# Optimization experiments

Measured on AMD Instinct MI355X. Metric: run time of the kernel, lower is better.

## Reference

```python
import jax, jax.numpy as jnp
import numpy as np

H = 32          # heads
E = 32          # head dim = mdl_channels // heads (must equal heads per module bug)
C = 1024        # mdl_channels == in_channels
MAXP = 128      # max_position_embeddings
EPS = 1e-5


def _layernorm(x, g, b):
    mu = jnp.mean(x, axis=-1, keepdims=True)
    var = jnp.var(x, axis=-1, keepdims=True)
    return (x - mu) * jax.lax.rsqrt(var + EPS) * g + b


def setup_inputs() -> dict:
    key = jax.random.key(0)
    ks = jax.random.split(key, 16)
    s = 0.02
    N, L = 4, 1024
    inp = {
        "x": jax.random.normal(ks[0], (N, L, C), jnp.float32),
        "Wq": jax.random.normal(ks[1], (C, C), jnp.float32) * s,
        "bq": jnp.zeros((C,), jnp.float32),
        "Wk": jax.random.normal(ks[2], (C, C), jnp.float32) * s,
        "bk": jnp.zeros((C,), jnp.float32),
        "Wv": jax.random.normal(ks[3], (C, C), jnp.float32) * s,
        "bv": jnp.zeros((C,), jnp.float32),
        "dist_emb": jax.random.normal(ks[4], (2 * MAXP + 1, E), jnp.float32) * s,
        "ln1_g": jnp.ones((C,), jnp.float32),
        "ln1_b": jnp.zeros((C,), jnp.float32),
        "ln2_g": jnp.ones((C,), jnp.float32),
        "ln2_b": jnp.zeros((C,), jnp.float32),
        "W1": jax.random.normal(ks[5], (C, C), jnp.float32) * s,
        "b1": jnp.zeros((C,), jnp.float32),
        "W2": jax.random.normal(ks[6], (C, C), jnp.float32) * s,
        "b2": jnp.zeros((C,), jnp.float32),
    }
    return inp


def reference(x, Wq, bq, Wk, bk, Wv, bv, dist_emb, ln1_g, ln1_b,
              ln2_g, ln2_b, W1, b1, W2, b2):
    N, L, _ = x.shape
    # QKV projections -> (N, L, H, E)
    q = (x @ Wq + bq).reshape(N, L, H, E)
    k = (x @ Wk + bk).reshape(N, L, H, E)
    v = (x @ Wv + bv).reshape(N, L, H, E)

    temp = 1.0 / np.sqrt(E).astype(np.float32)
    # content scores (N, H, L, S)
    QK = jnp.einsum('nlhe,nshe->nhls', q, k)
    # relative position scores (disentangled attention)
    pos = jnp.arange(L)
    dist = jnp.clip(pos[:, None] - pos[None, :], -MAXP, MAXP) + MAXP  # (L, L)
    pe = dist_emb[dist]                                              # (L, L, E)
    QK = QK + jnp.einsum('nlhe,lse->nhls', q, pe) \
            + jnp.einsum('nshe,lse->nhls', k, pe)
    A = jax.nn.softmax(temp * QK, axis=-1)          # dropout: eval mode (identity)
    t = jnp.einsum('nhls,nshe->nlhe', A, v).reshape(N, L, C)

    h = _layernorm(t + x, ln1_g, ln1_b)             # AddNorm (attention)
    m = jax.nn.relu(h @ W1 + b1) @ W2 + b2          # 2-layer MLP
    out = _layernorm(m + h, ln2_g, ln2_b)           # AddNorm (mlp)
    return jnp.swapaxes(out, 0, 1)                  # 'n f c -> f n c'
```

## Files before the change

### kernel.cpp

```cpp
#include <hip/hip_runtime.h>

#define H_ 32
#define E_ 32
#define C_ 1024
#define L_ 1024
#define N_ 4
#define M_ 4096
#define NH_ 128
#define D_ 257
#define QDP 264
#define TEMP_ 0.17677669529663687f
#define QSCALE_ (TEMP_ * 1.4426950408889634f)

typedef unsigned short u16;
typedef __attribute__((ext_vector_type(8))) short short8;
typedef __attribute__((ext_vector_type(4))) float f32x4;
typedef __attribute__((ext_vector_type(4))) unsigned short u16x4;

__device__ __forceinline__ u16 f2bf(float f) {
  union { float f; unsigned u; } v; v.f = f;
  unsigned r = v.u + 0x7fffu + ((v.u >> 16) & 1u);
  return (u16)(r >> 16);
}
__device__ __forceinline__ float bf2f(u16 h) {
  union { unsigned u; float f; } v; v.u = ((unsigned)h) << 16;
  return v.f;
}
__device__ __forceinline__ f32x4 mfma16(short8 a, short8 b, f32x4 c) {
  return __builtin_amdgcn_mfma_f32_16x16x32_bf16(a, b, c, 0, 0, 0);
}
__device__ __forceinline__ float exp2a(float x) {
  float r;
  asm("v_exp_f32 %0, %1\n\ts_nop 1" : "=v"(r) : "v"(x));
  return r;
}
__device__ __forceinline__ void gld16(const u16* g, u16* l) {
  __builtin_amdgcn_global_load_lds(
      (const __attribute__((address_space(1))) unsigned int*)g,
      (__attribute__((address_space(3))) unsigned int*)l, 16, 0, 0);
}

__global__ __launch_bounds__(256) void prep_kernel(
    const float* __restrict__ demb, const float* __restrict__ bq,
    const float* __restrict__ bk, const float* __restrict__ bv,
    u16* __restrict__ demb_b, float* __restrict__ bqkv) {
  int i = blockIdx.x * 256 + threadIdx.x;
  if (i < D_ * E_) demb_b[i] = f2bf(demb[i]);
  if (i < C_) { bqkv[i] = bq[i]; bqkv[C_ + i] = bk[i]; bqkv[2 * C_ + i] = bv[i]; }
}

__global__ __launch_bounds__(256) void cvt_x_kernel(const float* __restrict__ x,
                                                    u16* __restrict__ xb) {
  int i = blockIdx.x * 256 + threadIdx.x;
  f32x4 v = reinterpret_cast<const f32x4*>(x)[i];
  u16x4 o2;
  o2[0] = f2bf(v[0]); o2[1] = f2bf(v[1]); o2[2] = f2bf(v[2]); o2[3] = f2bf(v[3]);
  reinterpret_cast<u16x4*>(xb)[i] = o2;
}

__global__ __launch_bounds__(256) void transpose_w_kernel(const float* __restrict__ in,
                                                          u16* __restrict__ out) {
  __shared__ float tile[32][33];
  int j0 = blockIdx.x * 32, c0 = blockIdx.y * 32;
#pragma unroll
  for (int i = 0; i < 4; ++i) {
    int cy = threadIdx.y + i * 8;
    tile[cy][threadIdx.x] = in[(size_t)(c0 + cy) * C_ + j0 + threadIdx.x];
  }
  __syncthreads();
#pragma unroll
  for (int i = 0; i < 4; ++i) {
    int jy = threadIdx.y + i * 8;
    out[(size_t)(j0 + jy) * C_ + c0 + threadIdx.x] = f2bf(tile[threadIdx.x][jy]);
  }
}

template <int EPI>
__global__ __launch_bounds__(256) void gemm128_kernel(
    const u16* __restrict__ A, const u16* __restrict__ Bt, int K,
    const float* __restrict__ bias,
    u16* __restrict__ out0, u16* __restrict__ out1, u16* __restrict__ out2) {
  __shared__ u16 As[128 * 64];
  __shared__ u16 Bs[128 * 64];
  const int bid = blockIdx.x;
  const int m0 = (bid & 31) << 7;
  const int n0 = (bid >> 5) << 7;
  const int tid = threadIdx.x;
  const int w = tid >> 6, lane = tid & 63, lhi = lane >> 4, llo = lane & 15;
  const int wr = w >> 1, wc = w & 1;
  const int w4 = w << 2;
  const int srow = lane >> 3, scol = (lane & 7) << 3;
  f32x4 acc[4][4] = {};
  for (int k0 = 0; k0 < K; k0 += 64) {
#pragma unroll
    for (int j = 0; j < 4; ++j) {
      const int seg = w4 + j;
      const int row = (seg << 3) + srow;
      gld16(&A[(size_t)(m0 + row) * K + k0 + scol], &As[seg << 9]);
      gld16(&Bt[(size_t)(n0 + row) * K + k0 + scol], &Bs[seg << 9]);
    }
    __syncthreads();
#pragma unroll
    for (int kk = 0; kk < 2; ++kk) {
      const int ko = (kk << 5) + lhi * 8;
      short8 af[4], bf[4];
#pragma unroll
      for (int mi = 0; mi < 4; ++mi)
        af[mi] = *reinterpret_cast<const short8*>(&As[(wr * 64 + mi * 16 + llo) * 64 + ko]);
#pragma unroll
      for (int ni = 0; ni < 4; ++ni)
        bf[ni] = *reinterpret_cast<const short8*>(&Bs[(wc * 64 + ni * 16 + llo) * 64 + ko]);
#pragma unroll
      for (int mi = 0; mi < 4; ++mi)
#pragma unroll
        for (int ni = 0; ni < 4; ++ni)
          acc[mi][ni] = mfma16(af[mi], bf[ni], acc[mi][ni]);
    }
    __syncthreads();
  }
#pragma unroll
  for (int mi = 0; mi < 4; ++mi)
#pragma unroll
    for (int ni = 0; ni < 4; ++ni)
#pragma unroll
      for (int r = 0; r < 4; ++r) {
        int row = m0 + wr * 64 + mi * 16 + lhi * 4 + r;
        int col = n0 + wc * 64 + ni * 16 + llo;
        float v = acc[mi][ni][r] + bias[col];
        if constexpr (EPI == 0) {
          int which = col >> 10, jj = col & 1023, h = jj >> 5, e2 = jj & 31;
          int n = row >> 10, l = row & 1023;
          int nh = (n << 5) | h;
          if (which == 0) v *= QSCALE_;
          u16 bvv = f2bf(v);
          if (which == 0)      out0[((size_t)((nh << 10) | l)) * 32 + e2] = bvv;
          else if (which == 1) out1[((size_t)((nh << 10) | l)) * 32 + e2] = bvv;
          else                 out2[(((size_t)(nh * 32 + e2)) << 10) | l] = bvv;
        } else if constexpr (EPI == 1) {
          out0[(size_t)row * C_ + col] = f2bf(fmaxf(v, 0.f));
        } else {
          out0[(size_t)row * C_ + col] = f2bf(v);
        }
      }
}

__global__ __launch_bounds__(256) void qdkd_kernel(
    const u16* __restrict__ src, const u16* __restrict__ demb,
    u16* __restrict__ dst, int dstride, float scale,
    u16* __restrict__ aux0, u16* __restrict__ aux256) {
  const int wt = blockIdx.x * 4 + (threadIdx.x >> 6);
  const int lane = threadIdx.x & 63, lhi = lane >> 4, llo = lane & 15;
  const int m0 = wt << 4;
  short8 a = *reinterpret_cast<const short8*>(&src[(size_t)(m0 + llo) * E_ + lhi * 8]);
#pragma unroll
  for (int ct = 0; ct < 17; ++ct) {
    int d = ct * 16 + llo;
    short8 b = {0, 0, 0, 0, 0, 0, 0, 0};
    if (d < D_) b = *reinterpret_cast<const short8*>(&demb[d * E_ + lhi * 8]);
    f32x4 c = {};
    c = mfma16(a, b, c);
    if (d < D_) {
#pragma unroll
      for (int r = 0; r < 4; ++r) {
        u16 val = f2bf(c[r] * scale);
        dst[(size_t)(m0 + lhi * 4 + r) * dstride + d] = val;
        if (aux0 != nullptr && d == 0)     aux0[m0 + lhi * 4 + r] = val;
        if (aux256 != nullptr && d == 256) aux256[m0 + lhi * 4 + r] = val;
      }
    }
  }
}

__global__ __launch_bounds__(256) void attn_kernel(
    const u16* __restrict__ qw, const u16* __restrict__ kw,
    const u16* __restrict__ vT, const u16* __restrict__ QDg,
    const u16* __restrict__ KDg, const u16* __restrict__ kd0a,
    const u16* __restrict__ kd256a, u16* __restrict__ tb) {
  __shared__ u16 QDs[64 * QDP];
  __shared__ u16 kdc[2 * 1024];
  __shared__ u16 Pbuf[4 * 16 * 40];
  __shared__ float Lred[64];
  const int bid = blockIdx.x;
  const int nh = bid >> 4;
  const int l0 = (bid & 15) << 6;
  const int tid = threadIdx.x;
  const int w = tid >> 6, lane = tid & 63, lhi = lane >> 4, llo = lane & 15;
  const int lw0 = l0 + (w << 4);

  const u16* qb  = qw + (size_t)nh * (L_ * E_);
  const u16* kb  = kw + (size_t)nh * (L_ * E_);
  const u16* vb  = vT + (size_t)nh * (E_ * L_);
  const u16* qdg = QDg + (size_t)nh * ((size_t)L_ * QDP);
  const u16* kdg = KDg + (size_t)nh * ((size_t)L_ * D_);

  {
    const int rr = tid >> 2, q4 = tid & 3;
#pragma unroll
    for (int j = 0; j < 9; ++j) {
      int c = q4 + j * 4;
      if (c < 33)
        *reinterpret_cast<short8*>(&QDs[rr * QDP + c * 8]) =
            *reinterpret_cast<const short8*>(&qdg[(size_t)(l0 + rr) * QDP + c * 8]);
    }
    const int side = tid >> 7, off = (tid & 127) * 8;
    const u16* srcA = (side ? kd256a : kd0a) + (size_t)nh * L_ + off;
    *reinterpret_cast<short8*>(&kdc[side * 1024 + off]) =
        *reinterpret_cast<const short8*>(srcA);
  }
  __syncthreads();

  const short8 qA = *reinterpret_cast<const short8*>(&qb[(size_t)(lw0 + llo) * E_ + lhi * 8]);
  const int qr4 = (w << 4) + (lhi << 2);
  float qdf0[4], qdf256[4];
#pragma unroll
  for (int r = 0; r < 4; ++r) {
    qdf0[r]   = bf2f(QDs[(qr4 + r) * QDP + 0]);
    qdf256[r] = bf2f(QDs[(qr4 + r) * QDP + 256]);
  }

  u16* Pw = &Pbuf[w * 16 * 40];
  f32x4 o0 = {}, o1 = {};
  float lacc[4] = {0.f, 0.f, 0.f, 0.f};

  for (int s0 = 0; s0 < L_; s0 += 32) {
    short8 kB0 = *reinterpret_cast<const short8*>(&kb[(size_t)(s0 + llo) * E_ + lhi * 8]);
    short8 kB1 = *reinterpret_cast<const short8*>(&kb[(size_t)(s0 + 16 + llo) * E_ + lhi * 8]);
    f32x4 st0 = {}, st1 = {};
    st0 = mfma16(qA, kB0, st0);
    st1 = mfma16(qA, kB1, st1);

    const int dmin = lw0 - s0 - 31, dmax = lw0 + 15 - s0;
    float p0[4], p1[4];
    if (dmin >= 128 || dmax <= -128) {
      const int sd = (dmin >= 128) ? 1 : 0;
      const float* qdf = sd ? qdf256 : qdf0;
      const float kc0 = bf2f(kdc[sd * 1024 + s0 + llo]);
      const float kc1 = bf2f(kdc[sd * 1024 + s0 + 16 + llo]);
#pragma unroll
      for (int r = 0; r < 4; ++r) {
        p0[r] = exp2a(st0[r] + qdf[r] + kc0);
        p1[r] = exp2a(st1[r] + qdf[r] + kc1);
      }
    } else if (dmin >= -128 && dmax <= 128) {
      const int sc0 = s0 + llo, sc1 = s0 + 16 + llo;
      u16x4 kd0v = *reinterpret_cast<const u16x4*>(&kdg[256 * sc0 + lw0 + (lhi << 2) + 128]);
      u16x4 kd1v = *reinterpret_cast<const u16x4*>(&kdg[256 * sc1 + lw0 + (lhi << 2) + 128]);
#pragma unroll
      for (int r = 0; r < 4; ++r) {
        const int qq = lw0 + (lhi << 2) + r;
        float qd0 = bf2f(QDs[(qr4 + r) * QDP + (qq - sc0 + 128)]);
        float qd1 = bf2f(QDs[(qr4 + r) * QDP + (qq - sc1 + 128)]);
        p0[r] = exp2a(st0[r] + qd0 + bf2f(kd0v[r]));
        p1[r] = exp2a(st1[r] + qd1 + bf2f(kd1v[r]));
      }
    } else {
#pragma unroll
      for (int r = 0; r < 4; ++r) {
        const int qq = lw0 + (lhi << 2) + r;
        int d0 = qq - (s0 + llo);
        d0 = (d0 < -128 ? -128 : (d0 > 128 ? 128 : d0)) + 128;
        int d1 = qq - (s0 + 16 + llo);
        d1 = (d1 < -128 ? -128 : (d1 > 128 ? 128 : d1)) + 128;
        float qd0 = bf2f(QDs[(qr4 + r) * QDP + d0]);
        float qd1 = bf2f(QDs[(qr4 + r) * QDP + d1]);
        float kd0 = bf2f(kdg[(size_t)(s0 + llo) * D_ + d0]);
        float kd1 = bf2f(kdg[(size_t)(s0 + 16 + llo) * D_ + d1]);
        p0[r] = exp2a(st0[r] + qd0 + kd0);
        p1[r] = exp2a(st1[r] + qd1 + kd1);
      }
    }

#pragma unroll
    for (int r = 0; r < 4; ++r) {
      lacc[r] += p0[r] + p1[r];
      union { float f; unsigned u; } a0, a1; a0.f = p0[r]; a1.f = p1[r];
      const int prow = ((lhi << 2) + r) * 40;
      Pw[prow + llo]      = (u16)((a0.u + 0x8000u) >> 16);
      Pw[prow + 16 + llo] = (u16)((a1.u + 0x8000u) >> 16);
    }
    short8 pB = *reinterpret_cast<const short8*>(&Pw[llo * 40 + lhi * 8]);
    short8 vA0 = *reinterpret_cast<const short8*>(&vb[(size_t)llo * L_ + s0 + lhi * 8]);
    short8 vA1 = *reinterpret_cast<const short8*>(&vb[(size_t)(16 + llo) * L_ + s0 + lhi * 8]);
    o0 = mfma16(vA0, pB, o0);
    o1 = mfma16(vA1, pB, o1);
  }

#pragma unroll
  for (int r = 0; r < 4; ++r) {
    float t = lacc[r];
    t += __shfl_xor(t, 1); t += __shfl_xor(t, 2);
    t += __shfl_xor(t, 4); t += __shfl_xor(t, 8);
    if (llo == 0) Lred[(w << 4) + (lhi << 2) + r] = t;
  }
  const float inv = 1.0f / Lred[(w << 4) + llo];

  const int n = nh >> 5, h = nh & 31;
  const size_t obase = (((size_t)((n << 10) | (lw0 + llo))) * 32 + h) * 32;
  u16x4 w0, w1;
#pragma unroll
  for (int r = 0; r < 4; ++r) {
    w0[r] = f2bf(o0[r] * inv);
    w1[r] = f2bf(o1[r] * inv);
  }
  *reinterpret_cast<u16x4*>(&tb[obase + (lhi << 2)]) = w0;
  *reinterpret_cast<u16x4*>(&tb[obase + 16 + (lhi << 2)]) = w1;
}

__global__ __launch_bounds__(256) void ln1_kernel(
    const u16* __restrict__ tbuf, const float* __restrict__ x,
    const float* __restrict__ g, const float* __restrict__ b,
    u16* __restrict__ hb) {
  __shared__ float red[8];
  const int row = blockIdx.x, tid = threadIdx.x;
  const size_t base = (size_t)row * C_ + tid * 4;
  f32x4 xv = *reinterpret_cast<const f32x4*>(&x[base]);
  u16x4 tv = *reinterpret_cast<const u16x4*>(&tbuf[base]);
  float v[4]; float s1 = 0.f, s2 = 0.f;
#pragma unroll
  for (int i = 0; i < 4; ++i) {
    v[i] = xv[i] + bf2f(tv[i]);
    s1 += v[i]; s2 += v[i] * v[i];
  }
#pragma unroll
  for (int off = 32; off >= 1; off >>= 1) {
    s1 += __shfl_xor(s1, off); s2 += __shfl_xor(s2, off);
  }
  if ((tid & 63) == 0) { red[tid >> 6] = s1; red[4 + (tid >> 6)] = s2; }
  __syncthreads();
  float S1 = red[0] + red[1] + red[2] + red[3];
  float S2 = red[4] + red[5] + red[6] + red[7];
  float mu = S1 * (1.f / C_);
  float rs = rsqrtf(S2 * (1.f / C_) - mu * mu + 1e-5f);
#pragma unroll
  for (int i = 0; i < 4; ++i) {
    int c = tid * 4 + i;
    hb[base + i] = f2bf((v[i] - mu) * rs * g[c] + b[c]);
  }
}

__global__ __launch_bounds__(256) void ln2_kernel(
    const u16* __restrict__ mb, const u16* __restrict__ hb,
    const float* __restrict__ g, const float* __restrict__ b,
    float* __restrict__ out) {
  __shared__ float red[8];
  const int row = blockIdx.x, tid = threadIdx.x;
  const size_t base = (size_t)row * C_ + tid * 4;
  u16x4 mv = *reinterpret_cast<const u16x4*>(&mb[base]);
  u16x4 hv = *reinterpret_cast<const u16x4*>(&hb[base]);
  float v[4]; float s1 = 0.f, s2 = 0.f;
#pragma unroll
  for (int i = 0; i < 4; ++i) {
    v[i] = bf2f(mv[i]) + bf2f(hv[i]);
    s1 += v[i]; s2 += v[i] * v[i];
  }
#pragma unroll
  for (int off = 32; off >= 1; off >>= 1) {
    s1 += __shfl_xor(s1, off); s2 += __shfl_xor(s2, off);
  }
  if ((tid & 63) == 0) { red[tid >> 6] = s1; red[4 + (tid >> 6)] = s2; }
  __syncthreads();
  float S1 = red[0] + red[1] + red[2] + red[3];
  float S2 = red[4] + red[5] + red[6] + red[7];
  float mu = S1 * (1.f / C_);
  float rs = rsqrtf(S2 * (1.f / C_) - mu * mu + 1e-5f);
  const int n = row >> 10, l = row & 1023;
  const size_t ob = (size_t)(l * N_ + n) * C_ + tid * 4;
#pragma unroll
  for (int i = 0; i < 4; ++i) {
    int c = tid * 4 + i;
    out[ob + i] = (v[i] - mu) * rs * g[c] + b[c];
  }
}

extern "C" void kernel_launch(void* const* d_in, const int* in_sizes, int n_in,
                              void* d_out, int out_size, void* d_ws, size_t ws_size,
                              hipStream_t stream) {
  const float* x    = (const float*)d_in[0];
  const float* Wq   = (const float*)d_in[1];
  const float* bq   = (const float*)d_in[2];
  const float* Wk   = (const float*)d_in[3];
  const float* bk   = (const float*)d_in[4];
  const float* Wv   = (const float*)d_in[5];
  const float* bv   = (const float*)d_in[6];
  const float* demb = (const float*)d_in[7];
  const float* g1   = (const float*)d_in[8];
  const float* b1ln = (const float*)d_in[9];
  const float* g2   = (const float*)d_in[10];
  const float* b2ln = (const float*)d_in[11];
  const float* W1   = (const float*)d_in[12];
  const float* b1   = (const float*)d_in[13];
  const float* W2   = (const float*)d_in[14];
  const float* b2   = (const float*)d_in[15];
  float* outp = (float*)d_out;

  size_t o = 0;
  auto alloc = [&](size_t bytes) { size_t r = o; o += (bytes + 255) & ~(size_t)255; return r; };
  const size_t xb_o    = alloc((size_t)M_ * C_ * 2);
  const size_t wqkv_o  = alloc((size_t)3 * C_ * C_ * 2);
  const size_t w1_o    = alloc((size_t)C_ * C_ * 2);
  const size_t w2_o    = alloc((size_t)C_ * C_ * 2);
  const size_t bqkv_o  = alloc((size_t)3 * C_ * 4);
  const size_t demb_o  = alloc((size_t)D_ * E_ * 2);
  const size_t q_o     = alloc((size_t)NH_ * L_ * E_ * 2);
  const size_t k_o     = alloc((size_t)NH_ * L_ * E_ * 2);
  const size_t vt_o    = alloc((size_t)NH_ * L_ * E_ * 2);
  const size_t qd_o    = alloc((size_t)NH_ * L_ * QDP * 2);
  const size_t kd_o    = alloc((size_t)NH_ * L_ * D_ * 2);
  const size_t kd0_o   = alloc((size_t)NH_ * L_ * 2);
  const size_t kd256_o = alloc((size_t)NH_ * L_ * 2);
  const size_t t_o     = alloc((size_t)M_ * C_ * 2);
  const size_t h_o     = alloc((size_t)M_ * C_ * 2);
  const size_t m1_o    = alloc((size_t)M_ * C_ * 2);
  const size_t m_o     = alloc((size_t)M_ * C_ * 2);
  if (o > ws_size) return;

  char* ws = (char*)d_ws;
  u16*   xb     = (u16*)(ws + xb_o);
  u16*   wqkv_t = (u16*)(ws + wqkv_o);
  u16*   w1_t   = (u16*)(ws + w1_o);
  u16*   w2_t   = (u16*)(ws + w2_o);
  float* bqkv   = (float*)(ws + bqkv_o);
  u16*   demb_b = (u16*)(ws + demb_o);
  u16*   q_ws   = (u16*)(ws + q_o);
  u16*   k_ws   = (u16*)(ws + k_o);
  u16*   vT_ws  = (u16*)(ws + vt_o);
  u16*   QD     = (u16*)(ws + qd_o);
  u16*   KD     = (u16*)(ws + kd_o);
  u16*   kd0a   = (u16*)(ws + kd0_o);
  u16*   kd256a = (u16*)(ws + kd256_o);
  u16*   t_b16  = (u16*)(ws + t_o);
  u16*   h_b16  = (u16*)(ws + h_o);
  u16*   m1_b16 = (u16*)(ws + m1_o);
  u16*   m_b16  = (u16*)(ws + m_o);

  prep_kernel<<<33, 256, 0, stream>>>(demb, bq, bk, bv, demb_b, bqkv);
  cvt_x_kernel<<<(M_ * C_) / 1024, 256, 0, stream>>>(x, xb);
  dim3 tb_(32, 8), tg_(32, 32);
  transpose_w_kernel<<<tg_, tb_, 0, stream>>>(Wq, wqkv_t);
  transpose_w_kernel<<<tg_, tb_, 0, stream>>>(Wk, wqkv_t + (size_t)C_ * C_);
  transpose_w_kernel<<<tg_, tb_, 0, stream>>>(Wv, wqkv_t + (size_t)2 * C_ * C_);
  transpose_w_kernel<<<tg_, tb_, 0, stream>>>(W1, w1_t);
  transpose_w_kernel<<<tg_, tb_, 0, stream>>>(W2, w2_t);

  gemm128_kernel<0><<<32 * 24, 256, 0, stream>>>(xb, wqkv_t, C_, bqkv, q_ws, k_ws, vT_ws);

  qdkd_kernel<<<2048, 256, 0, stream>>>(q_ws, demb_b, QD, QDP, 1.0f, nullptr, nullptr);
  qdkd_kernel<<<2048, 256, 0, stream>>>(k_ws, demb_b, KD, D_, QSCALE_, kd0a, kd256a);

  attn_kernel<<<NH_ * 16, 256, 0, stream>>>(q_ws, k_ws, vT_ws, QD, KD, kd0a, kd256a, t_b16);

  ln1_kernel<<<M_, 256, 0, stream>>>(t_b16, x, g1, b1ln, h_b16);

  gemm128_kernel<1><<<32 * 8, 256, 0, stream>>>(h_b16, w1_t, C_, b1, m1_b16, nullptr, nullptr);
  gemm128_kernel<2><<<32 * 8, 256, 0, stream>>>(m1_b16, w2_t, C_, b2, m_b16, nullptr, nullptr);

  ln2_kernel<<<M_, 256, 0, stream>>>(m_b16, h_b16, g2, b2ln, outp);
}
```

Before: 321.7 us.

## Fuse Q·demb into attention, merge prep kernels, interleave key columns

New measurement: 311.8 us. 3.1% less time.

```diff
diff --git a/kernel.cpp b/kernel.cpp
--- a/kernel.cpp
+++ b/kernel.cpp
@@ -8,6 +8,7 @@
 #define M_ 4096
 #define NH_ 128
 #define D_ 257
+#define DPAD 272
 #define QDP 264
 #define TEMP_ 0.17677669529663687f
 #define QSCALE_ (TEMP_ * 1.4426950408889634f)
@@ -29,10 +30,14 @@
 __device__ __forceinline__ f32x4 mfma16(short8 a, short8 b, f32x4 c) {
   return __builtin_amdgcn_mfma_f32_16x16x32_bf16(a, b, c, 0, 0, 0);
 }
-__device__ __forceinline__ float exp2a(float x) {
+__device__ __forceinline__ float ex2(float x) {
+#if __has_builtin(__builtin_amdgcn_exp2f)
+  return __builtin_amdgcn_exp2f(x);
+#else
   float r;
   asm("v_exp_f32 %0, %1\n\ts_nop 1" : "=v"(r) : "v"(x));
   return r;
+#endif
 }
 __device__ __forceinline__ void gld16(const u16* g, u16* l) {
   __builtin_amdgcn_global_load_lds(
@@ -40,27 +45,33 @@
       (__attribute__((address_space(3))) unsigned int*)l, 16, 0, 0);
 }
 
-__global__ __launch_bounds__(256) void prep_kernel(
-    const float* __restrict__ demb, const float* __restrict__ bq,
-    const float* __restrict__ bk, const float* __restrict__ bv,
+__global__ __launch_bounds__(256) void misc_kernel(
+    const float* __restrict__ x, const float* __restrict__ demb,
+    const float* __restrict__ bq, const float* __restrict__ bk,
+    const float* __restrict__ bv, u16* __restrict__ xb,
     u16* __restrict__ demb_b, float* __restrict__ bqkv) {
-  int i = blockIdx.x * 256 + threadIdx.x;
-  if (i < D_ * E_) demb_b[i] = f2bf(demb[i]);
-  if (i < C_) { bqkv[i] = bq[i]; bqkv[C_ + i] = bk[i]; bqkv[2 * C_ + i] = bv[i]; }
-}
-
-__global__ __launch_bounds__(256) void cvt_x_kernel(const float* __restrict__ x,
-                                                    u16* __restrict__ xb) {
-  int i = blockIdx.x * 256 + threadIdx.x;
-  f32x4 v = reinterpret_cast<const f32x4*>(x)[i];
-  u16x4 o2;
-  o2[0] = f2bf(v[0]); o2[1] = f2bf(v[1]); o2[2] = f2bf(v[2]); o2[3] = f2bf(v[3]);
-  reinterpret_cast<u16x4*>(xb)[i] = o2;
-}
-
-__global__ __launch_bounds__(256) void transpose_w_kernel(const float* __restrict__ in,
-                                                          u16* __restrict__ out) {
+  const int b = blockIdx.x, tid = threadIdx.x;
+  if (b < 4096) {
+    int i = b * 256 + tid;
+    f32x4 v = reinterpret_cast<const f32x4*>(x)[i];
+    u16x4 o2;
+    o2[0] = f2bf(v[0]); o2[1] = f2bf(v[1]); o2[2] = f2bf(v[2]); o2[3] = f2bf(v[3]);
+    reinterpret_cast<u16x4*>(xb)[i] = o2;
+  } else {
+    int i = (b - 4096) * 256 + tid;
+    if (i < DPAD * E_) demb_b[i] = (i < D_ * E_) ? f2bf(demb[i]) : (u16)0;
+    if (i < C_) { bqkv[i] = bq[i]; bqkv[C_ + i] = bk[i]; bqkv[2 * C_ + i] = bv[i]; }
+  }
+}
+
+__global__ __launch_bounds__(256) void transpose_w_kernel(
+    const float* __restrict__ Wq, const float* __restrict__ Wk,
+    const float* __restrict__ Wv, const float* __restrict__ W1,
+    const float* __restrict__ W2, u16* __restrict__ out_base) {
   __shared__ float tile[32][33];
+  const int z = blockIdx.z;
+  const float* in = (z == 0) ? Wq : (z == 1) ? Wk : (z == 2) ? Wv : (z == 3) ? W1 : W2;
+  u16* out = out_base + (size_t)z * C_ * C_;
   int j0 = blockIdx.x * 32, c0 = blockIdx.y * 32;
 #pragma unroll
   for (int i = 0; i < 4; ++i) {
@@ -146,8 +157,7 @@
 
 __global__ __launch_bounds__(256) void qdkd_kernel(
     const u16* __restrict__ src, const u16* __restrict__ demb,
-    u16* __restrict__ dst, int dstride, float scale,
-    u16* __restrict__ aux0, u16* __restrict__ aux256) {
+    u16* __restrict__ dst, u16* __restrict__ aux0, u16* __restrict__ aux256) {
   const int wt = blockIdx.x * 4 + (threadIdx.x >> 6);
   const int lane = threadIdx.x & 63, lhi = lane >> 4, llo = lane & 15;
   const int m0 = wt << 4;
@@ -162,10 +172,10 @@
     if (d < D_) {
 #pragma unroll
       for (int r = 0; r < 4; ++r) {
-        u16 val = f2bf(c[r] * scale);
-        dst[(size_t)(m0 + lhi * 4 + r) * dstride + d] = val;
-        if (aux0 != nullptr && d == 0)     aux0[m0 + lhi * 4 + r] = val;
-        if (aux256 != nullptr && d == 256) aux256[m0 + lhi * 4 + r] = val;
+        u16 val = f2bf(c[r] * QSCALE_);
+        dst[(size_t)(m0 + lhi * 4 + r) * D_ + d] = val;
+        if (d == 0)   aux0[m0 + lhi * 4 + r] = val;
+        if (d == 256) aux256[m0 + lhi * 4 + r] = val;
       }
     }
   }
@@ -173,7 +183,7 @@
 
 __global__ __launch_bounds__(256) void attn_kernel(
     const u16* __restrict__ qw, const u16* __restrict__ kw,
-    const u16* __restrict__ vT, const u16* __restrict__ QDg,
+    const u16* __restrict__ vT, const u16* __restrict__ dembp,
     const u16* __restrict__ KDg, const u16* __restrict__ kd0a,
     const u16* __restrict__ kd256a, u16* __restrict__ tb) {
   __shared__ u16 QDs[64 * QDP];
@@ -181,8 +191,8 @@
   __shared__ u16 Pbuf[4 * 16 * 40];
   __shared__ float Lred[64];
   const int bid = blockIdx.x;
-  const int nh = bid >> 4;
-  const int l0 = (bid & 15) << 6;
+  const int nh = bid & (NH_ - 1);
+  const int l0 = (bid >> 7) << 6;
   const int tid = threadIdx.x;
   const int w = tid >> 6, lane = tid & 63, lhi = lane >> 4, llo = lane & 15;
   const int lw0 = l0 + (w << 4);
@@ -190,26 +200,29 @@
   const u16* qb  = qw + (size_t)nh * (L_ * E_);
   const u16* kb  = kw + (size_t)nh * (L_ * E_);
   const u16* vb  = vT + (size_t)nh * (E_ * L_);
-  const u16* qdg = QDg + (size_t)nh * ((size_t)L_ * QDP);
   const u16* kdg = KDg + (size_t)nh * ((size_t)L_ * D_);
 
   {
-    const int rr = tid >> 2, q4 = tid & 3;
-#pragma unroll
-    for (int j = 0; j < 9; ++j) {
-      int c = q4 + j * 4;
-      if (c < 33)
-        *reinterpret_cast<short8*>(&QDs[rr * QDP + c * 8]) =
-            *reinterpret_cast<const short8*>(&qdg[(size_t)(l0 + rr) * QDP + c * 8]);
-    }
     const int side = tid >> 7, off = (tid & 127) * 8;
     const u16* srcA = (side ? kd256a : kd0a) + (size_t)nh * L_ + off;
     *reinterpret_cast<short8*>(&kdc[side * 1024 + off]) =
         *reinterpret_cast<const short8*>(srcA);
   }
+
+  const short8 qA = *reinterpret_cast<const short8*>(&qb[(size_t)(lw0 + llo) * E_ + lhi * 8]);
+
+#pragma unroll
+  for (int dt = 0; dt < 17; ++dt) {
+    short8 db = *reinterpret_cast<const short8*>(&dembp[(dt * 16 + llo) * E_ + lhi * 8]);
+    f32x4 qd = {};
+    qd = mfma16(qA, db, qd);
+    const int qrow = (w << 4) + (lhi << 2);
+#pragma unroll
+    for (int r = 0; r < 4; ++r)
+      QDs[(qrow + r) * QDP + dt * 16 + llo] = f2bf(qd[r]);
+  }
   __syncthreads();
 
-  const short8 qA = *reinterpret_cast<const short8*>(&qb[(size_t)(lw0 + llo) * E_ + lhi * 8]);
   const int qr4 = (w << 4) + (lhi << 2);
   float qdf0[4], qdf256[4];
 #pragma unroll
@@ -223,8 +236,9 @@
   float lacc[4] = {0.f, 0.f, 0.f, 0.f};
 
   for (int s0 = 0; s0 < L_; s0 += 32) {
-    short8 kB0 = *reinterpret_cast<const short8*>(&kb[(size_t)(s0 + llo) * E_ + lhi * 8]);
-    short8 kB1 = *reinterpret_cast<const short8*>(&kb[(size_t)(s0 + 16 + llo) * E_ + lhi * 8]);
+    const int se = s0 + 2 * llo;
+    short8 kB0 = *reinterpret_cast<const short8*>(&kb[(size_t)se * E_ + lhi * 8]);
+    short8 kB1 = *reinterpret_cast<const short8*>(&kb[(size_t)(se + 1) * E_ + lhi * 8]);
     f32x4 st0 = {}, st1 = {};
     st0 = mfma16(qA, kB0, st0);
     st1 = mfma16(qA, kB1, st1);
@@ -234,49 +248,47 @@
     if (dmin >= 128 || dmax <= -128) {
       const int sd = (dmin >= 128) ? 1 : 0;
       const float* qdf = sd ? qdf256 : qdf0;
-      const float kc0 = bf2f(kdc[sd * 1024 + s0 + llo]);
-      const float kc1 = bf2f(kdc[sd * 1024 + s0 + 16 + llo]);
+      unsigned kc2 = *reinterpret_cast<const unsigned*>(&kdc[sd * 1024 + se]);
+      const float kc0 = bf2f((u16)kc2), kc1 = bf2f((u16)(kc2 >> 16));
 #pragma unroll
       for (int r = 0; r < 4; ++r) {
-        p0[r] = exp2a(st0[r] + qdf[r] + kc0);
-        p1[r] = exp2a(st1[r] + qdf[r] + kc1);
+        p0[r] = ex2(st0[r] + qdf[r] + kc0);
+        p1[r] = ex2(st1[r] + qdf[r] + kc1);
       }
     } else if (dmin >= -128 && dmax <= 128) {
-      const int sc0 = s0 + llo, sc1 = s0 + 16 + llo;
-      u16x4 kd0v = *reinterpret_cast<const u16x4*>(&kdg[256 * sc0 + lw0 + (lhi << 2) + 128]);
-      u16x4 kd1v = *reinterpret_cast<const u16x4*>(&kdg[256 * sc1 + lw0 + (lhi << 2) + 128]);
+      const int qoff = lw0 + (lhi << 2) + 128;
+      u16x4 kd0v = *reinterpret_cast<const u16x4*>(&kdg[256 * se + qoff]);
+      u16x4 kd1v = *reinterpret_cast<const u16x4*>(&kdg[256 * (se + 1) + qoff]);
 #pragma unroll
       for (int r = 0; r < 4; ++r) {
         const int qq = lw0 + (lhi << 2) + r;
-        float qd0 = bf2f(QDs[(qr4 + r) * QDP + (qq - sc0 + 128)]);
-        float qd1 = bf2f(QDs[(qr4 + r) * QDP + (qq - sc1 + 128)]);
-        p0[r] = exp2a(st0[r] + qd0 + bf2f(kd0v[r]));
-        p1[r] = exp2a(st1[r] + qd1 + bf2f(kd1v[r]));
+        float qd0 = bf2f(QDs[(qr4 + r) * QDP + (qq - se + 128)]);
+        float qd1 = bf2f(QDs[(qr4 + r) * QDP + (qq - se + 127)]);
+        p0[r] = ex2(st0[r] + qd0 + bf2f(kd0v[r]));
+        p1[r] = ex2(st1[r] + qd1 + bf2f(kd1v[r]));
       }
     } else {
 #pragma unroll
       for (int r = 0; r < 4; ++r) {
         const int qq = lw0 + (lhi << 2) + r;
-        int d0 = qq - (s0 + llo);
+        int d0 = qq - se;
         d0 = (d0 < -128 ? -128 : (d0 > 128 ? 128 : d0)) + 128;
-        int d1 = qq - (s0 + 16 + llo);
+        int d1 = qq - se - 1;
         d1 = (d1 < -128 ? -128 : (d1 > 128 ? 128 : d1)) + 128;
         float qd0 = bf2f(QDs[(qr4 + r) * QDP + d0]);
         float qd1 = bf2f(QDs[(qr4 + r) * QDP + d1]);
-        float kd0 = bf2f(kdg[(size_t)(s0 + llo) * D_ + d0]);
-        float kd1 = bf2f(kdg[(size_t)(s0 + 16 + llo) * D_ + d1]);
-        p0[r] = exp2a(st0[r] + qd0 + kd0);
-        p1[r] = exp2a(st1[r] + qd1 + kd1);
+        float kd0 = bf2f(kdg[(size_t)se * D_ + d0]);
+        float kd1 = bf2f(kdg[(size_t)(se + 1) * D_ + d1]);
+        p0[r] = ex2(st0[r] + qd0 + kd0);
+        p1[r] = ex2(st1[r] + qd1 + kd1);
       }
     }
 
 #pragma unroll
     for (int r = 0; r < 4; ++r) {
       lacc[r] += p0[r] + p1[r];
-      union { float f; unsigned u; } a0, a1; a0.f = p0[r]; a1.f = p1[r];
-      const int prow = ((lhi << 2) + r) * 40;
-      Pw[prow + llo]      = (u16)((a0.u + 0x8000u) >> 16);
-      Pw[prow + 16 + llo] = (u16)((a1.u + 0x8000u) >> 16);
+      unsigned pw = (unsigned)f2bf(p0[r]) | ((unsigned)f2bf(p1[r]) << 16);
+      *reinterpret_cast<unsigned*>(&Pw[((lhi << 2) + r) * 40 + 2 * llo]) = pw;
     }
     short8 pB = *reinterpret_cast<const short8*>(&Pw[llo * 40 + lhi * 8]);
     short8 vA0 = *reinterpret_cast<const short8*>(&vb[(size_t)llo * L_ + s0 + lhi * 8]);
@@ -400,11 +412,10 @@
   const size_t w1_o    = alloc((size_t)C_ * C_ * 2);
   const size_t w2_o    = alloc((size_t)C_ * C_ * 2);
   const size_t bqkv_o  = alloc((size_t)3 * C_ * 4);
-  const size_t demb_o  = alloc((size_t)D_ * E_ * 2);
+  const size_t demb_o  = alloc((size_t)DPAD * E_ * 2);
   const size_t q_o     = alloc((size_t)NH_ * L_ * E_ * 2);
   const size_t k_o     = alloc((size_t)NH_ * L_ * E_ * 2);
   const size_t vt_o    = alloc((size_t)NH_ * L_ * E_ * 2);
-  const size_t qd_o    = alloc((size_t)NH_ * L_ * QDP * 2);
   const size_t kd_o    = alloc((size_t)NH_ * L_ * D_ * 2);
   const size_t kd0_o   = alloc((size_t)NH_ * L_ * 2);
   const size_t kd256_o = alloc((size_t)NH_ * L_ * 2);
@@ -424,7 +435,6 @@
   u16*   q_ws   = (u16*)(ws + q_o);
   u16*   k_ws   = (u16*)(ws + k_o);
   u16*   vT_ws  = (u16*)(ws + vt_o);
-  u16*   QD     = (u16*)(ws + qd_o);
   u16*   KD     = (u16*)(ws + kd_o);
   u16*   kd0a   = (u16*)(ws + kd0_o);
   u16*   kd256a = (u16*)(ws + kd256_o);
@@ -433,21 +443,15 @@
   u16*   m1_b16 = (u16*)(ws + m1_o);
   u16*   m_b16  = (u16*)(ws + m_o);
 
-  prep_kernel<<<33, 256, 0, stream>>>(demb, bq, bk, bv, demb_b, bqkv);
-  cvt_x_kernel<<<(M_ * C_) / 1024, 256, 0, stream>>>(x, xb);
-  dim3 tb_(32, 8), tg_(32, 32);
-  transpose_w_kernel<<<tg_, tb_, 0, stream>>>(Wq, wqkv_t);
-  transpose_w_kernel<<<tg_, tb_, 0, stream>>>(Wk, wqkv_t + (size_t)C_ * C_);
-  transpose_w_kernel<<<tg_, tb_, 0, stream>>>(Wv, wqkv_t + (size_t)2 * C_ * C_);
-  transpose_w_kernel<<<tg_, tb_, 0, stream>>>(W1, w1_t);
-  transpose_w_kernel<<<tg_, tb_, 0, stream>>>(W2, w2_t);
+  misc_kernel<<<4096 + 34, 256, 0, stream>>>(x, demb, bq, bk, bv, xb, demb_b, bqkv);
+  dim3 tb_(32, 8), tg_(32, 32, 5);
+  transpose_w_kernel<<<tg_, tb_, 0, stream>>>(Wq, Wk, Wv, W1, W2, wqkv_t);
 
   gemm128_kernel<0><<<32 * 24, 256, 0, stream>>>(xb, wqkv_t, C_, bqkv, q_ws, k_ws, vT_ws);
 
-  qdkd_kernel<<<2048, 256, 0, stream>>>(q_ws, demb_b, QD, QDP, 1.0f, nullptr, nullptr);
-  qdkd_kernel<<<2048, 256, 0, stream>>>(k_ws, demb_b, KD, D_, QSCALE_, kd0a, kd256a);
-
-  attn_kernel<<<NH_ * 16, 256, 0, stream>>>(q_ws, k_ws, vT_ws, QD, KD, kd0a, kd256a, t_b16);
+  qdkd_kernel<<<2048, 256, 0, stream>>>(k_ws, demb_b, KD, kd0a, kd256a);
+
+  attn_kernel<<<NH_ * 16, 256, 0, stream>>>(q_ws, k_ws, vT_ws, demb_b, KD, kd0a, kd256a, t_b16);
 
   ln1_kernel<<<M_, 256, 0, stream>>>(t_b16, x, g1, b1ln, h_b16);
 
```
